# Optimization experiments

Measured on AMD Instinct MI355X. Metric: run time of the kernel, lower is better.

The kernel has to match this reference:

```python
import jax, jax.numpy as jnp
import numpy as np

H, I, E, TOPK = 1024, 4096, 8, 2
B, S = 2, 2048


def setup_inputs() -> dict:
    key = jax.random.key(0)
    ks = jax.random.split(key, 6)
    x = jax.random.normal(ks[0], (B, S, H), dtype=jnp.float32)
    expert_indices = jax.random.randint(ks[1], (B, S, TOPK), 0, E)
    expert_weights = jax.random.uniform(ks[2], (B, S, TOPK), dtype=jnp.float32)
    gate_proj = jax.random.normal(ks[3], (E, I, H), dtype=jnp.float32) * 0.02
    up_proj = jax.random.normal(ks[4], (E, I, H), dtype=jnp.float32) * 0.02
    down_proj = jax.random.normal(ks[5], (E, H, I), dtype=jnp.float32) * 0.02
    return {"x": x, "expert_indices": expert_indices, "expert_weights": expert_weights,
            "gate_proj": gate_proj, "up_proj": up_proj, "down_proj": down_proj}


def reference(x, expert_indices, expert_weights, gate_proj, up_proj, down_proj):
    b, s, h = x.shape
    xf = x.reshape(-1, h)                      # [T, H]
    ei = expert_indices.reshape(-1, expert_indices.shape[-1])   # [T, K]
    ew = expert_weights.reshape(-1, expert_weights.shape[-1])   # [T, K]
    n_experts = gate_proj.shape[0]
    out = jnp.zeros_like(xf)
    for e in range(n_experts):
        # combined routing weight of this expert per token (sum over topk slots)
        w_e = jnp.sum(jnp.where(ei == e, ew, 0.0), axis=-1)     # [T]
        g = xf @ gate_proj[e].T                # [T, I]
        u = xf @ up_proj[e].T                  # [T, I]
        inter = jax.nn.silu(g) * u             # fused SiLU*mul
        out = out + w_e[:, None] * (inter @ down_proj[e].T)     # weighted scatter-add
    return out.reshape(b, s, h)
```

## Files before the change

kernel.cpp:

```cpp
#include <hip/hip_runtime.h>
#include <cstdint>
#include <cstddef>

#define H_DIM 1024
#define I_DIM 4096
#define E_NUM 8
#define TOPK  2
#define T_NUM 4096
#define NROWS (T_NUM * TOPK)
#define BK    32

typedef _Float16 half8 __attribute__((ext_vector_type(8)));
typedef float    f32x4 __attribute__((ext_vector_type(4)));

__device__ __forceinline__ void async_copy16(void* lds, const void* g)
{
    __builtin_amdgcn_global_load_lds(
        (__attribute__((address_space(1))) unsigned int*)g,
        (__attribute__((address_space(3))) unsigned int*)lds,
        16 , 0 , 0 );
}

__global__ void cvt_f32_to_f16(const float* __restrict__ s, _Float16* __restrict__ d, int n4)
{
    int i = blockIdx.x * blockDim.x + threadIdx.x;
    if (i >= n4) return;
    float4 v = reinterpret_cast<const float4*>(s)[i];
    union { _Float16 h[4]; unsigned long long u; } o;
    o.h[0] = (_Float16)v.x; o.h[1] = (_Float16)v.y;
    o.h[2] = (_Float16)v.z; o.h[3] = (_Float16)v.w;
    reinterpret_cast<unsigned long long*>(d)[i] = o.u;
}

__global__ void route_count(const int* __restrict__ ei, int* __restrict__ counts)
{
    int s = blockIdx.x * blockDim.x + threadIdx.x;
    if (s < NROWS) atomicAdd(&counts[ei[s]], 1);
}

__global__ void route_scatter(const int* __restrict__ ei, const float* __restrict__ ew,
                              const int* __restrict__ counts, int* __restrict__ offs,
                              int* __restrict__ token_of_row, float* __restrict__ weight_of_row)
{
    __shared__ int cur[E_NUM];
    if (threadIdx.x == 0) {
        int acc = 0;
        for (int e = 0; e < E_NUM; ++e) { offs[e] = acc; cur[e] = acc; acc += counts[e]; }
        offs[E_NUM] = acc;
    }
    __syncthreads();
    for (int s = (int)threadIdx.x; s < NROWS; s += (int)blockDim.x) {
        int e = ei[s];
        int r = atomicAdd(&cur[e], 1);
        token_of_row[r]  = s >> 1;
        weight_of_row[r] = ew[s];
    }
}

__global__ __launch_bounds__(256) void gateup_gemm(
    const _Float16* __restrict__ xh,
    const _Float16* __restrict__ Wg,
    const _Float16* __restrict__ Wu,
    const int*      __restrict__ token_of_row,
    const int*      __restrict__ offs,
    _Float16*       __restrict__ inter)
{
    const int e = blockIdx.z;
    const int seg_start = offs[e], seg_end = offs[e + 1];
    const int m0 = seg_start + (int)blockIdx.y * 128;
    if (m0 >= seg_end) return;
    const int n0 = (int)blockIdx.x * 64;

    __shared__ _Float16 Ash[128 * BK];
    __shared__ _Float16 Bgs[64 * BK];
    __shared__ _Float16 Bus[64 * BK];

    const int tid  = (int)threadIdx.x;
    const int lane = tid & 63, wid = tid >> 6;
    const int wm = wid >> 1, wn = wid & 1;

    const int c  = lane & 3;
    const int rl = lane >> 2;

    const _Float16* pA[2];
    _Float16* lA[2];
#pragma unroll
    for (int j = 0; j < 2; ++j) {
        int q = 2 * wid + j;
        int r = m0 + q * 16 + rl;
        if (r > seg_end - 1) r = seg_end - 1;
        int tok = token_of_row[r];
        pA[j] = xh + (size_t)tok * H_DIM + c * 8;
        lA[j] = &Ash[q * 16 * BK];
    }
    const int brow = wid * 16 + rl;
    const _Float16* pBg = Wg + ((size_t)e * I_DIM + n0 + brow) * H_DIM + c * 8;
    const _Float16* pBu = Wu + ((size_t)e * I_DIM + n0 + brow) * H_DIM + c * 8;
    _Float16* lBg = &Bgs[wid * 16 * BK];
    _Float16* lBu = &Bus[wid * 16 * BK];

    f32x4 accg[4][2], accu[4][2];
#pragma unroll
    for (int i = 0; i < 4; ++i)
#pragma unroll
        for (int j = 0; j < 2; ++j) {
            accg[i][j] = (f32x4){0.f, 0.f, 0.f, 0.f};
            accu[i][j] = (f32x4){0.f, 0.f, 0.f, 0.f};
        }

    const int fm = lane & 15, fk = (lane >> 4) * 8;

    for (int kt = 0; kt < H_DIM / BK; ++kt) {
        const int ko = kt * BK;
        __syncthreads();
        async_copy16(lA[0], pA[0] + ko);
        async_copy16(lA[1], pA[1] + ko);
        async_copy16(lBg,   pBg   + ko);
        async_copy16(lBu,   pBu   + ko);
        __syncthreads();

        half8 a[4], bg[2], bu[2];
#pragma unroll
        for (int i = 0; i < 4; ++i)
            a[i] = *(const half8*)&Ash[(wm * 64 + i * 16 + fm) * BK + fk];
#pragma unroll
        for (int j = 0; j < 2; ++j) {
            bg[j] = *(const half8*)&Bgs[(wn * 32 + j * 16 + fm) * BK + fk];
            bu[j] = *(const half8*)&Bus[(wn * 32 + j * 16 + fm) * BK + fk];
        }
#pragma unroll
        for (int i = 0; i < 4; ++i)
#pragma unroll
            for (int j = 0; j < 2; ++j) {
                accg[i][j] = __builtin_amdgcn_mfma_f32_16x16x32_f16(a[i], bg[j], accg[i][j], 0, 0, 0);
                accu[i][j] = __builtin_amdgcn_mfma_f32_16x16x32_f16(a[i], bu[j], accu[i][j], 0, 0, 0);
            }
    }

#pragma unroll
    for (int i = 0; i < 4; ++i) {
#pragma unroll
        for (int reg = 0; reg < 4; ++reg) {
            int r = m0 + wm * 64 + i * 16 + (lane >> 4) * 4 + reg;
            if (r < seg_end) {
#pragma unroll
                for (int j = 0; j < 2; ++j) {
                    int col = n0 + wn * 32 + j * 16 + fm;
                    float g = accg[i][j][reg];
                    float u = accu[i][j][reg];
                    float sv = (g / (1.f + __expf(-g))) * u;
                    inter[(size_t)r * I_DIM + col] = (_Float16)sv;
                }
            }
        }
    }
}

__global__ __launch_bounds__(256) void down_gemm(
    const _Float16* __restrict__ inter,
    const _Float16* __restrict__ Wd,
    const int*      __restrict__ token_of_row,
    const float*    __restrict__ weight_of_row,
    const int*      __restrict__ offs,
    float*          __restrict__ out)
{
    const int e = blockIdx.z;
    const int seg_start = offs[e], seg_end = offs[e + 1];
    const int m0 = seg_start + (int)blockIdx.y * 128;
    if (m0 >= seg_end) return;
    const int n0 = (int)blockIdx.x * 128;

    __shared__ _Float16 Ash[128 * BK];
    __shared__ _Float16 Bsh[128 * BK];

    const int tid  = (int)threadIdx.x;
    const int lane = tid & 63, wid = tid >> 6;
    const int wm = wid >> 1, wn = wid & 1;
    const int c = lane & 3, rl = lane >> 2;

    const _Float16* pA[2]; _Float16* lA[2];
    const _Float16* pB[2]; _Float16* lB[2];
#pragma unroll
    for (int j = 0; j < 2; ++j) {
        int q = 2 * wid + j;
        int row_in = q * 16 + rl;
        int r = m0 + row_in;
        if (r > seg_end - 1) r = seg_end - 1;
        pA[j] = inter + (size_t)r * I_DIM + c * 8;
        lA[j] = &Ash[q * 16 * BK];
        int n = n0 + row_in;
        pB[j] = Wd + ((size_t)e * H_DIM + n) * I_DIM + c * 8;
        lB[j] = &Bsh[q * 16 * BK];
    }

    f32x4 acc[4][4];
#pragma unroll
    for (int i = 0; i < 4; ++i)
#pragma unroll
        for (int j = 0; j < 4; ++j) acc[i][j] = (f32x4){0.f, 0.f, 0.f, 0.f};

    const int fm = lane & 15, fk = (lane >> 4) * 8;

    for (int kt = 0; kt < I_DIM / BK; ++kt) {
        const int ko = kt * BK;
        __syncthreads();
        async_copy16(lA[0], pA[0] + ko);
        async_copy16(lA[1], pA[1] + ko);
        async_copy16(lB[0], pB[0] + ko);
        async_copy16(lB[1], pB[1] + ko);
        __syncthreads();

        half8 a[4], b[4];
#pragma unroll
        for (int i = 0; i < 4; ++i)
            a[i] = *(const half8*)&Ash[(wm * 64 + i * 16 + fm) * BK + fk];
#pragma unroll
        for (int j = 0; j < 4; ++j)
            b[j] = *(const half8*)&Bsh[(wn * 64 + j * 16 + fm) * BK + fk];
#pragma unroll
        for (int i = 0; i < 4; ++i)
#pragma unroll
            for (int j = 0; j < 4; ++j)
                acc[i][j] = __builtin_amdgcn_mfma_f32_16x16x32_f16(a[i], b[j], acc[i][j], 0, 0, 0);
    }

#pragma unroll
    for (int i = 0; i < 4; ++i) {
#pragma unroll
        for (int reg = 0; reg < 4; ++reg) {
            int r = m0 + wm * 64 + i * 16 + (lane >> 4) * 4 + reg;
            if (r < seg_end) {
                float w = weight_of_row[r];
                int   t = token_of_row[r];
#pragma unroll
                for (int j = 0; j < 4; ++j) {
                    int col = n0 + wn * 64 + j * 16 + fm;
                    atomicAdd(&out[(size_t)t * H_DIM + col], w * acc[i][j][reg]);
                }
            }
        }
    }
}

extern "C" void kernel_launch(void* const* d_in, const int* in_sizes, int n_in,
                              void* d_out, int out_size, void* d_ws, size_t ws_size,
                              hipStream_t stream)
{
    const float* x  = (const float*)d_in[0];
    const int*   ei = (const int*)  d_in[1];
    const float* ew = (const float*)d_in[2];
    const float* gp = (const float*)d_in[3];
    const float* up = (const float*)d_in[4];
    const float* dp = (const float*)d_in[5];
    float* out = (float*)d_out;

    char* ws = (char*)d_ws;
    size_t o = 0;
    _Float16* xh    = (_Float16*)(ws + o); o += (size_t)T_NUM * H_DIM * 2;
    _Float16* Wg_h  = (_Float16*)(ws + o); o += (size_t)E_NUM * I_DIM * H_DIM * 2;
    _Float16* Wu_h  = (_Float16*)(ws + o); o += (size_t)E_NUM * I_DIM * H_DIM * 2;
    _Float16* Wd_h  = (_Float16*)(ws + o); o += (size_t)E_NUM * I_DIM * H_DIM * 2;
    _Float16* inter = (_Float16*)(ws + o); o += (size_t)NROWS * I_DIM * 2;
    int*   counts        = (int*)  (ws + o);
    int*   offs          = (int*)  (ws + o + 64);
    int*   token_of_row  = (int*)  (ws + o + 256);
    float* weight_of_row = (float*)(ws + o + 256 + (size_t)NROWS * 4);
    size_t ws_need = o + 256 + (size_t)NROWS * 8;
    if (ws_size < ws_need) return;

    hipMemsetAsync(counts, 0, 64, stream);
    hipMemsetAsync(d_out, 0, (size_t)out_size * sizeof(float), stream);

    const int nt = 256;
    const int nx = T_NUM * H_DIM / 4;
    cvt_f32_to_f16<<<(nx + nt - 1) / nt, nt, 0, stream>>>(x, xh, nx);
    const int nw = E_NUM * I_DIM * H_DIM / 4;
    cvt_f32_to_f16<<<(nw + nt - 1) / nt, nt, 0, stream>>>(gp, Wg_h, nw);
    cvt_f32_to_f16<<<(nw + nt - 1) / nt, nt, 0, stream>>>(up, Wu_h, nw);
    cvt_f32_to_f16<<<(nw + nt - 1) / nt, nt, 0, stream>>>(dp, Wd_h, nw);

    route_count<<<NROWS / 256, 256, 0, stream>>>(ei, counts);
    route_scatter<<<1, 256, 0, stream>>>(ei, ew, counts, offs, token_of_row, weight_of_row);

    gateup_gemm<<<dim3(I_DIM / 64, NROWS / 128, E_NUM), 256, 0, stream>>>(
        xh, Wg_h, Wu_h, token_of_row, offs, inter);
    down_gemm<<<dim3(H_DIM / 128, NROWS / 128, E_NUM), 256, 0, stream>>>(
        inter, Wd_h, token_of_row, weight_of_row, offs, out);
}
```

Before: 773.0 us.

## Double K tile with XOR-swizzled LDS and fuse conversion and routing kernels

Raises the GEMM K-tile from 32 to 64 and adds an XOR swizzle to the LDS layout for both the gate/up and down GEMMs. This halves the number of barrier-separated loads per K loop and is meant to avoid LDS bank conflicts. It also merges the four f32-to-f16 conversion launches into one kernel, and merges the count and scatter routing kernels into one 1024-thread block, dropping a memset. The larger tiles double LDS use per block, which may reduce occupancy.

```diff
diff --git a/kernel.cpp b/kernel.cpp
--- a/kernel.cpp
+++ b/kernel.cpp
@@ -8,7 +8,7 @@
 #define TOPK  2
 #define T_NUM 4096
 #define NROWS (T_NUM * TOPK)
-#define BK    32
+#define BK    64
 
 typedef _Float16 half8 __attribute__((ext_vector_type(8)));
 typedef float    f32x4 __attribute__((ext_vector_type(4)));
@@ -21,35 +21,47 @@
         16 , 0 , 0 );
 }
 
-__global__ void cvt_f32_to_f16(const float* __restrict__ s, _Float16* __restrict__ d, int n4)
+
+#define NX4 (T_NUM * H_DIM / 4)
+#define NW4 (E_NUM * I_DIM * H_DIM / 4)
+__global__ void cvt_all(const float* __restrict__ x,  const float* __restrict__ gp,
+                        const float* __restrict__ up, const float* __restrict__ dp,
+                        _Float16* __restrict__ xh, _Float16* __restrict__ wg,
+                        _Float16* __restrict__ wu, _Float16* __restrict__ wd)
 {
     int i = blockIdx.x * blockDim.x + threadIdx.x;
-    if (i >= n4) return;
-    float4 v = reinterpret_cast<const float4*>(s)[i];
+    const int total = NX4 + 3 * NW4;
+    if (i >= total) return;
+    const float* s; _Float16* d; int j;
+    if (i < NX4)              { s = x;  d = xh; j = i; }
+    else if (i < NX4 + NW4)   { s = gp; d = wg; j = i - NX4; }
+    else if (i < NX4 + 2*NW4) { s = up; d = wu; j = i - NX4 - NW4; }
+    else                      { s = dp; d = wd; j = i - NX4 - 2*NW4; }
+    float4 v = reinterpret_cast<const float4*>(s)[j];
     union { _Float16 h[4]; unsigned long long u; } o;
     o.h[0] = (_Float16)v.x; o.h[1] = (_Float16)v.y;
     o.h[2] = (_Float16)v.z; o.h[3] = (_Float16)v.w;
-    reinterpret_cast<unsigned long long*>(d)[i] = o.u;
-}
-
-__global__ void route_count(const int* __restrict__ ei, int* __restrict__ counts)
-{
-    int s = blockIdx.x * blockDim.x + threadIdx.x;
-    if (s < NROWS) atomicAdd(&counts[ei[s]], 1);
-}
-
-__global__ void route_scatter(const int* __restrict__ ei, const float* __restrict__ ew,
-                              const int* __restrict__ counts, int* __restrict__ offs,
-                              int* __restrict__ token_of_row, float* __restrict__ weight_of_row)
-{
+    reinterpret_cast<unsigned long long*>(d)[j] = o.u;
+}
+
+__global__ void route_all(const int* __restrict__ ei, const float* __restrict__ ew,
+                          int* __restrict__ offs,
+                          int* __restrict__ token_of_row, float* __restrict__ weight_of_row)
+{
+    __shared__ int cnt[E_NUM];
     __shared__ int cur[E_NUM];
-    if (threadIdx.x == 0) {
+    const int t = (int)threadIdx.x;
+    if (t < E_NUM) cnt[t] = 0;
+    __syncthreads();
+    for (int s = t; s < NROWS; s += (int)blockDim.x) atomicAdd(&cnt[ei[s]], 1);
+    __syncthreads();
+    if (t == 0) {
         int acc = 0;
-        for (int e = 0; e < E_NUM; ++e) { offs[e] = acc; cur[e] = acc; acc += counts[e]; }
+        for (int e = 0; e < E_NUM; ++e) { offs[e] = acc; cur[e] = acc; acc += cnt[e]; }
         offs[E_NUM] = acc;
     }
     __syncthreads();
-    for (int s = (int)threadIdx.x; s < NROWS; s += (int)blockDim.x) {
+    for (int s = t; s < NROWS; s += (int)blockDim.x) {
         int e = ei[s];
         int r = atomicAdd(&cur[e], 1);
         token_of_row[r]  = s >> 1;
@@ -79,25 +91,32 @@
     const int lane = tid & 63, wid = tid >> 6;
     const int wm = wid >> 1, wn = wid & 1;
 
-    const int c  = lane & 3;
-    const int rl = lane >> 2;
-
-    const _Float16* pA[2];
-    _Float16* lA[2];
+    const int c  = lane & 7;
+    const int rl = lane >> 3;
+    const int gc = c ^ rl;
+
+    const _Float16* pA[4];
+    _Float16* lA[4];
+#pragma unroll
+    for (int j = 0; j < 4; ++j) {
+        int q = 4 * wid + j;
+        int r = m0 + q * 8 + rl;
+        if (r > seg_end - 1) r = seg_end - 1;
+        int tok = token_of_row[r];
+        pA[j] = xh + (size_t)tok * H_DIM + gc * 8;
+        lA[j] = &Ash[q * 8 * BK];
+    }
+    const _Float16* pBg[2]; const _Float16* pBu[2];
+    _Float16* lBg[2]; _Float16* lBu[2];
 #pragma unroll
     for (int j = 0; j < 2; ++j) {
         int q = 2 * wid + j;
-        int r = m0 + q * 16 + rl;
-        if (r > seg_end - 1) r = seg_end - 1;
-        int tok = token_of_row[r];
-        pA[j] = xh + (size_t)tok * H_DIM + c * 8;
-        lA[j] = &Ash[q * 16 * BK];
-    }
-    const int brow = wid * 16 + rl;
-    const _Float16* pBg = Wg + ((size_t)e * I_DIM + n0 + brow) * H_DIM + c * 8;
-    const _Float16* pBu = Wu + ((size_t)e * I_DIM + n0 + brow) * H_DIM + c * 8;
-    _Float16* lBg = &Bgs[wid * 16 * BK];
-    _Float16* lBu = &Bus[wid * 16 * BK];
+        int t = q * 8 + rl;
+        pBg[j] = Wg + ((size_t)e * I_DIM + n0 + t) * H_DIM + gc * 8;
+        pBu[j] = Wu + ((size_t)e * I_DIM + n0 + t) * H_DIM + gc * 8;
+        lBg[j] = &Bgs[q * 8 * BK];
+        lBu[j] = &Bus[q * 8 * BK];
+    }
 
     f32x4 accg[4][2], accu[4][2];
 #pragma unroll
@@ -108,40 +127,48 @@
             accu[i][j] = (f32x4){0.f, 0.f, 0.f, 0.f};
         }
 
-    const int fm = lane & 15, fk = (lane >> 4) * 8;
+    const int fm = lane & 15, kq = lane >> 4;
+    const int sw = fm & 7;
 
     for (int kt = 0; kt < H_DIM / BK; ++kt) {
         const int ko = kt * BK;
         __syncthreads();
-        async_copy16(lA[0], pA[0] + ko);
-        async_copy16(lA[1], pA[1] + ko);
-        async_copy16(lBg,   pBg   + ko);
-        async_copy16(lBu,   pBu   + ko);
+#pragma unroll
+        for (int j = 0; j < 4; ++j) async_copy16(lA[j], pA[j] + ko);
+#pragma unroll
+        for (int j = 0; j < 2; ++j) {
+            async_copy16(lBg[j], pBg[j] + ko);
+            async_copy16(lBu[j], pBu[j] + ko);
+        }
         __syncthreads();
 
-        half8 a[4], bg[2], bu[2];
-#pragma unroll
-        for (int i = 0; i < 4; ++i)
-            a[i] = *(const half8*)&Ash[(wm * 64 + i * 16 + fm) * BK + fk];
-#pragma unroll
-        for (int j = 0; j < 2; ++j) {
-            bg[j] = *(const half8*)&Bgs[(wn * 32 + j * 16 + fm) * BK + fk];
-            bu[j] = *(const half8*)&Bus[(wn * 32 + j * 16 + fm) * BK + fk];
-        }
-#pragma unroll
-        for (int i = 0; i < 4; ++i)
+#pragma unroll
+        for (int h = 0; h < 2; ++h) {
+            const int kc = h * 4 + kq;
+            half8 a[4], bg[2], bu[2];
+#pragma unroll
+            for (int i = 0; i < 4; ++i)
+                a[i] = *(const half8*)&Ash[(wm * 64 + i * 16 + fm) * BK + (kc ^ sw) * 8];
 #pragma unroll
             for (int j = 0; j < 2; ++j) {
-                accg[i][j] = __builtin_amdgcn_mfma_f32_16x16x32_f16(a[i], bg[j], accg[i][j], 0, 0, 0);
-                accu[i][j] = __builtin_amdgcn_mfma_f32_16x16x32_f16(a[i], bu[j], accu[i][j], 0, 0, 0);
+                bg[j] = *(const half8*)&Bgs[(wn * 32 + j * 16 + fm) * BK + (kc ^ sw) * 8];
+                bu[j] = *(const half8*)&Bus[(wn * 32 + j * 16 + fm) * BK + (kc ^ sw) * 8];
             }
+#pragma unroll
+            for (int i = 0; i < 4; ++i)
+#pragma unroll
+                for (int j = 0; j < 2; ++j) {
+                    accg[i][j] = __builtin_amdgcn_mfma_f32_16x16x32_f16(a[i], bg[j], accg[i][j], 0, 0, 0);
+                    accu[i][j] = __builtin_amdgcn_mfma_f32_16x16x32_f16(a[i], bu[j], accu[i][j], 0, 0, 0);
+                }
+        }
     }
 
 #pragma unroll
     for (int i = 0; i < 4; ++i) {
 #pragma unroll
         for (int reg = 0; reg < 4; ++reg) {
-            int r = m0 + wm * 64 + i * 16 + (lane >> 4) * 4 + reg;
+            int r = m0 + wm * 64 + i * 16 + kq * 4 + reg;
             if (r < seg_end) {
 #pragma unroll
                 for (int j = 0; j < 2; ++j) {
@@ -176,21 +203,22 @@
     const int tid  = (int)threadIdx.x;
     const int lane = tid & 63, wid = tid >> 6;
     const int wm = wid >> 1, wn = wid & 1;
-    const int c = lane & 3, rl = lane >> 2;
-
-    const _Float16* pA[2]; _Float16* lA[2];
-    const _Float16* pB[2]; _Float16* lB[2];
-#pragma unroll
-    for (int j = 0; j < 2; ++j) {
-        int q = 2 * wid + j;
-        int row_in = q * 16 + rl;
-        int r = m0 + row_in;
+    const int c  = lane & 7;
+    const int rl = lane >> 3;
+    const int gc = c ^ rl;
+
+    const _Float16* pA[4]; _Float16* lA[4];
+    const _Float16* pB[4]; _Float16* lB[4];
+#pragma unroll
+    for (int j = 0; j < 4; ++j) {
+        int q = 4 * wid + j;
+        int t = q * 8 + rl;
+        int r = m0 + t;
         if (r > seg_end - 1) r = seg_end - 1;
-        pA[j] = inter + (size_t)r * I_DIM + c * 8;
-        lA[j] = &Ash[q * 16 * BK];
-        int n = n0 + row_in;
-        pB[j] = Wd + ((size_t)e * H_DIM + n) * I_DIM + c * 8;
-        lB[j] = &Bsh[q * 16 * BK];
+        pA[j] = inter + (size_t)r * I_DIM + gc * 8;
+        lA[j] = &Ash[q * 8 * BK];
+        pB[j] = Wd + ((size_t)e * H_DIM + n0 + t) * I_DIM + gc * 8;
+        lB[j] = &Bsh[q * 8 * BK];
     }
 
     f32x4 acc[4][4];
@@ -199,36 +227,42 @@
 #pragma unroll
         for (int j = 0; j < 4; ++j) acc[i][j] = (f32x4){0.f, 0.f, 0.f, 0.f};
 
-    const int fm = lane & 15, fk = (lane >> 4) * 8;
+    const int fm = lane & 15, kq = lane >> 4;
+    const int sw = fm & 7;
 
     for (int kt = 0; kt < I_DIM / BK; ++kt) {
         const int ko = kt * BK;
         __syncthreads();
-        async_copy16(lA[0], pA[0] + ko);
-        async_copy16(lA[1], pA[1] + ko);
-        async_copy16(lB[0], pB[0] + ko);
-        async_copy16(lB[1], pB[1] + ko);
+#pragma unroll
+        for (int j = 0; j < 4; ++j) {
+            async_copy16(lA[j], pA[j] + ko);
+            async_copy16(lB[j], pB[j] + ko);
+        }
         __syncthreads();
 
-        half8 a[4], b[4];
-#pragma unroll
-        for (int i = 0; i < 4; ++i)
-            a[i] = *(const half8*)&Ash[(wm * 64 + i * 16 + fm) * BK + fk];
-#pragma unroll
-        for (int j = 0; j < 4; ++j)
-            b[j] = *(const half8*)&Bsh[(wn * 64 + j * 16 + fm) * BK + fk];
-#pragma unroll
-        for (int i = 0; i < 4; ++i)
+#pragma unroll
+        for (int h = 0; h < 2; ++h) {
+            const int kc = h * 4 + kq;
+            half8 a[4], b[4];
+#pragma unroll
+            for (int i = 0; i < 4; ++i)
+                a[i] = *(const half8*)&Ash[(wm * 64 + i * 16 + fm) * BK + (kc ^ sw) * 8];
 #pragma unroll
             for (int j = 0; j < 4; ++j)
-                acc[i][j] = __builtin_amdgcn_mfma_f32_16x16x32_f16(a[i], b[j], acc[i][j], 0, 0, 0);
+                b[j] = *(const half8*)&Bsh[(wn * 64 + j * 16 + fm) * BK + (kc ^ sw) * 8];
+#pragma unroll
+            for (int i = 0; i < 4; ++i)
+#pragma unroll
+                for (int j = 0; j < 4; ++j)
+                    acc[i][j] = __builtin_amdgcn_mfma_f32_16x16x32_f16(a[i], b[j], acc[i][j], 0, 0, 0);
+        }
     }
 
 #pragma unroll
     for (int i = 0; i < 4; ++i) {
 #pragma unroll
         for (int reg = 0; reg < 4; ++reg) {
-            int r = m0 + wm * 64 + i * 16 + (lane >> 4) * 4 + reg;
+            int r = m0 + wm * 64 + i * 16 + kq * 4 + reg;
             if (r < seg_end) {
                 float w = weight_of_row[r];
                 int   t = token_of_row[r];
@@ -261,26 +295,19 @@
     _Float16* Wu_h  = (_Float16*)(ws + o); o += (size_t)E_NUM * I_DIM * H_DIM * 2;
     _Float16* Wd_h  = (_Float16*)(ws + o); o += (size_t)E_NUM * I_DIM * H_DIM * 2;
     _Float16* inter = (_Float16*)(ws + o); o += (size_t)NROWS * I_DIM * 2;
-    int*   counts        = (int*)  (ws + o);
-    int*   offs          = (int*)  (ws + o + 64);
+    int*   offs          = (int*)  (ws + o);
     int*   token_of_row  = (int*)  (ws + o + 256);
     float* weight_of_row = (float*)(ws + o + 256 + (size_t)NROWS * 4);
     size_t ws_need = o + 256 + (size_t)NROWS * 8;
     if (ws_size < ws_need) return;
 
-    hipMemsetAsync(counts, 0, 64, stream);
     hipMemsetAsync(d_out, 0, (size_t)out_size * sizeof(float), stream);
 
     const int nt = 256;
-    const int nx = T_NUM * H_DIM / 4;
-    cvt_f32_to_f16<<<(nx + nt - 1) / nt, nt, 0, stream>>>(x, xh, nx);
-    const int nw = E_NUM * I_DIM * H_DIM / 4;
-    cvt_f32_to_f16<<<(nw + nt - 1) / nt, nt, 0, stream>>>(gp, Wg_h, nw);
-    cvt_f32_to_f16<<<(nw + nt - 1) / nt, nt, 0, stream>>>(up, Wu_h, nw);
-    cvt_f32_to_f16<<<(nw + nt - 1) / nt, nt, 0, stream>>>(dp, Wd_h, nw);
-
-    route_count<<<NROWS / 256, 256, 0, stream>>>(ei, counts);
-    route_scatter<<<1, 256, 0, stream>>>(ei, ew, counts, offs, token_of_row, weight_of_row);
+    const int ncvt = NX4 + 3 * NW4;
+    cvt_all<<<(ncvt + nt - 1) / nt, nt, 0, stream>>>(x, gp, up, dp, xh, Wg_h, Wu_h, Wd_h);
+
+    route_all<<<1, 1024, 0, stream>>>(ei, ew, offs, token_of_row, weight_of_row);
 
     gateup_gemm<<<dim3(I_DIM / 64, NROWS / 128, E_NUM), 256, 0, stream>>>(
         xh, Wg_h, Wu_h, token_of_row, offs, inter);
```

Result: slower. 816.8 us (+5.7%).
